# Optimization experiments

Measured on AMD Instinct MI355X. Metric: run time of the kernel, lower is better.

## Reference

```python
import jax, jax.numpy as jnp
import numpy as np

TEMP = 0.1
GROUPS = 16
EPS = 1e-5
COS_EPS = 1e-8


def _encoder(x, conv_w, conv_b, gn_g, gn_b):
    # Conv2d(C,C,3,pad=1) -> GroupNorm(16,C) -> ReLU -> AdaptiveAvgPool2d(1) -> Flatten
    y = jax.lax.conv_general_dilated(
        x, conv_w, window_strides=(1, 1), padding='SAME',
        dimension_numbers=('NCHW', 'OIHW', 'NCHW')) + conv_b[None, :, None, None]
    B, C, H, W = y.shape
    yg = y.reshape(B, GROUPS, C // GROUPS, H, W)
    mu = yg.mean(axis=(2, 3, 4), keepdims=True)
    var = yg.var(axis=(2, 3, 4), keepdims=True)
    yn = ((yg - mu) * jax.lax.rsqrt(var + EPS)).reshape(B, C, H, W)
    y = yn * gn_g[None, :, None, None] + gn_b[None, :, None, None]
    y = jax.nn.relu(y)
    return y.mean(axis=(2, 3))  # [B, C]


def _projector(h, w1, b1, w2, b2, ln_g, ln_b):
    h = jax.nn.relu(h @ w1 + b1)
    h = h @ w2 + b2
    mu = h.mean(axis=-1, keepdims=True)
    var = h.var(axis=-1, keepdims=True)
    return (h - mu) * jax.lax.rsqrt(var + EPS) * ln_g + ln_b


def _predictor(z, w1, b1, w2, b2):
    return jax.nn.relu(z @ w1 + b1) @ w2 + b2


def _l2norm(z):
    n = jnp.sqrt(jnp.sum(z * z, axis=1, keepdims=True))
    return z / jnp.maximum(n, COS_EPS)


def _pair_loss(zi, zj, off_idx):
    # vectorized version of the nested-loop cosine-sim + cross-entropy (label 0)
    S = (_l2norm(zi) @ _l2norm(zj).T) / TEMP  # [B, B]
    pos = jnp.diagonal(S)                     # sim(i_k, j_k)
    neg = jnp.take_along_axis(S, off_idx, axis=1)  # [B, B-1], row k = S[k, l!=k]
    logits = jnp.concatenate([pos[:, None], neg], axis=1)
    return jnp.mean(jax.nn.logsumexp(logits, axis=1) - logits[:, 0])


def setup_inputs() -> dict:
    key = jax.random.key(0)
    ks = jax.random.split(key, 32)
    B, C, H, W, P = 256, 256, 16, 16, 128
    d = {}
    d['x_t2w'] = jax.random.normal(ks[0], (B, C, H, W), jnp.float32)
    d['x_t2f'] = jax.random.normal(ks[1], (B, C, H, W), jnp.float32)
    d['x_t1n'] = jax.random.normal(ks[2], (B, C, H, W), jnp.float32)
    i = 3
    for m in ('t2w', 't2f', 't1n'):
        d[f'conv_w_{m}'] = jax.random.normal(ks[i], (C, C, 3, 3), jnp.float32) * 0.02; i += 1
        d[f'conv_b_{m}'] = jnp.zeros((C,), jnp.float32)
        d[f'gn_g_{m}'] = jnp.ones((C,), jnp.float32)
        d[f'gn_b_{m}'] = jnp.zeros((C,), jnp.float32)
    d['proj_w1'] = jax.random.normal(ks[i], (C, C), jnp.float32) * 0.02; i += 1
    d['proj_b1'] = jnp.zeros((C,), jnp.float32)
    d['proj_w2'] = jax.random.normal(ks[i], (C, P), jnp.float32) * 0.02; i += 1
    d['proj_b2'] = jnp.zeros((P,), jnp.float32)
    d['ln_g'] = jnp.ones((P,), jnp.float32)
    d['ln_b'] = jnp.zeros((P,), jnp.float32)
    d['pred_w1'] = jax.random.normal(ks[i], (P, P), jnp.float32) * 0.02; i += 1
    d['pred_b1'] = jnp.zeros((P,), jnp.float32)
    d['pred_w2'] = jax.random.normal(ks[i], (P, P), jnp.float32) * 0.02; i += 1
    d['pred_b2'] = jnp.zeros((P,), jnp.float32)
    return d


def reference(x_t2w, x_t2f, x_t1n,
              conv_w_t2w, conv_b_t2w, gn_g_t2w, gn_b_t2w,
              conv_w_t2f, conv_b_t2f, gn_g_t2f, gn_b_t2f,
              conv_w_t1n, conv_b_t1n, gn_g_t1n, gn_b_t1n,
              proj_w1, proj_b1, proj_w2, proj_b2, ln_g, ln_b,
              pred_w1, pred_b1, pred_w2, pred_b2):
    xs = [x_t2w, x_t2f, x_t1n]
    enc_params = [(conv_w_t2w, conv_b_t2w, gn_g_t2w, gn_b_t2w),
                  (conv_w_t2f, conv_b_t2f, gn_g_t2f, gn_b_t2f),
                  (conv_w_t1n, conv_b_t1n, gn_g_t1n, gn_b_t1n)]
    encoded = [_encoder(x, *p) for x, p in zip(xs, enc_params)]
    projected = [_projector(e, proj_w1, proj_b1, proj_w2, proj_b2, ln_g, ln_b) for e in encoded]
    preds = [_predictor(z, pred_w1, pred_b1, pred_w2, pred_b2) for z in projected]

    B = projected[0].shape[0]
    off_idx = jnp.asarray(np.array([[l for l in range(B) if l != k] for k in range(B)],
                                    dtype=np.int32))
    pairs = [(0, 1), (0, 2), (1, 2)]
    loss = sum(_pair_loss(projected[i], projected[j], off_idx) for i, j in pairs) / len(pairs)

    return (jnp.stack(encoded), jnp.stack(projected), jnp.stack(preds), loss)
```

## Files before the change

kernel.cpp:

```cpp
#include <hip/hip_runtime.h>
#include <hip/hip_bf16.h>

typedef float f32x4 __attribute__((ext_vector_type(4)));
typedef __bf16 bf16x8 __attribute__((ext_vector_type(8)));
typedef unsigned short u16x8 __attribute__((ext_vector_type(8)));

#define GN_EPS 1e-5f
#define LN_EPS 1e-5f
#define COS_EPS_F 1e-8f

__device__ __forceinline__ unsigned short f2bf(float f) {
  unsigned int u = __builtin_bit_cast(unsigned int, f);
  u += 0x7fffu + ((u >> 16) & 1u);
  return (unsigned short)(u >> 16);
}

__global__ void transpose_kernel(const float* __restrict__ x0,
                                 const float* __restrict__ x1,
                                 const float* __restrict__ x2,
                                 unsigned short* __restrict__ xT,
                                 unsigned int strideElems, int mBase) {
  __shared__ float lds[64][129];
  int m = mBase + (blockIdx.x >> 11);
  int bid = blockIdx.x & 2047;
  const float* x = (m == 0) ? x0 : ((m == 1) ? x1 : x2);
  unsigned short* dst = xT + (unsigned int)(m - mBase) * strideElems;

  int hwt = bid & 3, cit = (bid >> 2) & 1, b = bid >> 3;
  int hw0 = hwt * 64, ci0 = cit * 128;
  int tid = threadIdx.x;

  int hwx = tid & 63, cy0 = tid >> 6;
  const float* xb = x + (b * 256 + ci0) * 256 + hw0;
  #pragma unroll 8
  for (int p = 0; p < 32; ++p) {
    int cy = cy0 + 4 * p;
    lds[hwx][cy] = xb[cy * 256 + hwx];
  }
  __syncthreads();

  int cp = tid & 63, hy0 = tid >> 6;
  unsigned int* outp = (unsigned int*)(dst + (b * 256 + hw0) * 256 + ci0);
  #pragma unroll 4
  for (int p = 0; p < 16; ++p) {
    int hy = hy0 + 4 * p;
    float lo = lds[hy][2 * cp];
    float hi = lds[hy][2 * cp + 1];
    unsigned int w = ((unsigned int)f2bf(hi) << 16) | f2bf(lo);
    outp[hy * 128 + cp] = w;
  }
}

__global__ void pack_kernel(const float* __restrict__ w0,
                            const float* __restrict__ w1,
                            const float* __restrict__ w2,
                            unsigned short* __restrict__ wp) {
  int m = blockIdx.y;
  const float* w = (m == 0) ? w0 : ((m == 1) ? w1 : w2);
  int idx = blockIdx.x * 256 + threadIdx.x;
  int ci = idx & 255;
  int rest = idx >> 8;
  int khw = rest % 9, co = rest / 9;
  wp[m * 589824 + idx] = f2bf(w[(co * 256 + ci) * 9 + khw]);
}

__device__ __forceinline__ void gl_lds16(const unsigned short* g, unsigned short* l) {
  __builtin_amdgcn_global_load_lds(
      (const __attribute__((address_space(1))) void*)g,
      (__attribute__((address_space(3))) void*)l, 16, 0, 0);
}

__launch_bounds__(512, 2)
__global__ void conv_gn_pool(const unsigned short* __restrict__ xT,
                             unsigned int xTstride,
                             const unsigned short* __restrict__ wp,
                             const float* __restrict__ cb0, const float* __restrict__ cb1,
                             const float* __restrict__ cb2,
                             const float* __restrict__ gg0, const float* __restrict__ gg1,
                             const float* __restrict__ gg2,
                             const float* __restrict__ gb0, const float* __restrict__ gb1,
                             const float* __restrict__ gb2,
                             float* __restrict__ enc, int mBase, int chunk) {
  __shared__ unsigned short As[2][16384];
  __shared__ unsigned short Bb[3][4096];
  __shared__ unsigned short zbuf[32];
  __shared__ float gsum[16], gsq[16], pooled[256];

  int bid = blockIdx.x;
  int xcd = bid & 7, kk = bid >> 3;
  int nt = kk & 1;
  int pg = xcd * chunk + (kk >> 1);
  int mm = mBase + (pg >> 7);
  int pr = pg & 127;

  const float* cbias = (mm == 0) ? cb0 : ((mm == 1) ? cb1 : cb2);
  const float* gng   = (mm == 0) ? gg0 : ((mm == 1) ? gg1 : gg2);
  const float* gnb   = (mm == 0) ? gb0 : ((mm == 1) ? gb1 : gb2);

  int tid = threadIdx.x;
  int wid = tid >> 6, lane = tid & 63;
  int wr = wid >> 1, wc = wid & 1;
  int l15 = lane & 15, l4 = lane >> 4;

  if (tid < 16) { gsum[tid] = 0.f; gsq[tid] = 0.f; }
  if (tid < 256) pooled[tid] = 0.f;
  if (tid < 32) zbuf[tid] = 0;

  const unsigned short* xbPair =
      xT + (unsigned int)(mm - mBase) * xTstride + (unsigned int)(pr * 2) * 65536u;
  const unsigned short* wpB = wp + mm * 589824 + (nt * 128) * 2304;

  int sco = tid >> 2, sk4 = tid & 3;

  int hh8[8], ww8[8], bq8[8];
  #pragma unroll
  for (int mf = 0; mf < 8; ++mf) {
    int r = wr * 128 + mf * 16 + l15;
    int img = r >> 8, p = r & 255;
    hh8[mf] = p >> 4; ww8[mf] = p & 15;
    bq8[mf] = img * 8192 + p * 32 + l4 * 8;
  }
  int bq4[4];
  #pragma unroll
  for (int nf = 0; nf < 4; ++nf)
    bq4[nf] = (wc * 64 + nf * 16 + l15) * 32 + l4 * 8;

  f32x4 acc[8][4];
  #pragma unroll
  for (int i = 0; i < 8; ++i)
    #pragma unroll
    for (int j = 0; j < 4; ++j) acc[i][j] = (f32x4)(0.0f);

  #define LD8(P) __builtin_bit_cast(bf16x8, *(const u16x8*)(P))

  #define STAGE_A(KCN, PAR)                                                    \
    {                                                                          \
      unsigned short* dstA = &As[(PAR)][0];                                    \
      _Pragma("unroll")                                                        \
      for (int j = 0; j < 4; ++j) {                                            \
        int c = tid + j * 512;                                                 \
        int img_ = c >> 10, p_ = (c >> 2) & 255, k4_ = c & 3;                  \
        gl_lds16(xbPair + img_ * 65536 + p_ * 256 + (KCN) * 32 + k4_ * 8,      \
                 dstA + c * 8);                                                \
      }                                                                        \
    }
  #define STAGE_B(KC2, TAP2, BUF2)                                             \
    gl_lds16(wpB + sco * 2304 + (TAP2) * 256 + (KC2) * 32 + sk4 * 8,           \
             &Bb[(BUF2)][tid * 8]);

  #define TAP_BODY(TAP, DH, DW, DO_A, DO_B, KC2, TAP2, VMN)                    \
    {                                                                          \
      if (DO_A) STAGE_A(kc + 1, (kc + 1) & 1);                                 \
      if (DO_B) STAGE_B(KC2, TAP2, ((TAP) + 2) % 3);                           \
      const unsigned short* AsC = &As[kc & 1][0];                              \
      bf16x8 af[8], bfr[4];                                                    \
      _Pragma("unroll")                                                        \
      for (int nf = 0; nf < 4; ++nf)                                           \
        bfr[nf] = LD8(&Bb[(TAP) % 3][bq4[nf]]);                                \
      _Pragma("unroll")                                                        \
      for (int mf = 0; mf < 8; ++mf) {                                         \
        int ok = 1;                                                            \
        if ((DH) == 0) ok &= (hh8[mf] >= 1);                                   \
        if ((DH) == 2) ok &= (hh8[mf] <= 14);                                  \
        if ((DW) == 0) ok &= (ww8[mf] >= 1);                                   \
        if ((DW) == 2) ok &= (ww8[mf] <= 14);                                  \
        const unsigned short* pa =                                             \
            ok ? AsC + (bq8[mf] + (((DH) * 16 + (DW)) - 17) * 32)              \
               : &zbuf[l4 * 8];                                                \
        af[mf] = LD8(pa);                                                      \
      }                                                                        \
      __builtin_amdgcn_s_barrier();                                            \
      asm volatile("s_waitcnt lgkmcnt(0)" ::: "memory");                       \
      __builtin_amdgcn_sched_barrier(0);                                       \
      __builtin_amdgcn_s_setprio(1);                                           \
      _Pragma("unroll")                                                        \
      for (int mf = 0; mf < 8; ++mf)                                           \
        _Pragma("unroll")                                                      \
        for (int nf = 0; nf < 4; ++nf)                                         \
          acc[mf][nf] = __builtin_amdgcn_mfma_f32_16x16x32_bf16(               \
              af[mf], bfr[nf], acc[mf][nf], 0, 0, 0);                          \
      __builtin_amdgcn_s_setprio(0);                                           \
      asm volatile("s_waitcnt vmcnt(" #VMN ")" ::: "memory");                  \
      __builtin_amdgcn_s_barrier();                                            \
    }

  {
    int kc = 0; (void)kc;
    STAGE_A(0, 0);
    STAGE_B(0, 0, 0);
    STAGE_B(0, 1, 1);
    asm volatile("s_waitcnt vmcnt(1)" ::: "memory");
    __builtin_amdgcn_s_barrier();
  }

  for (int kc = 0; kc < 7; ++kc) {
    TAP_BODY(0, 0, 0, 1, 1, kc, 2, 5)
    TAP_BODY(1, 0, 1, 0, 1, kc, 3, 1)
    TAP_BODY(2, 0, 2, 0, 1, kc, 4, 1)
    TAP_BODY(3, 1, 0, 0, 1, kc, 5, 1)
    TAP_BODY(4, 1, 1, 0, 1, kc, 6, 1)
    TAP_BODY(5, 1, 2, 0, 1, kc, 7, 1)
    TAP_BODY(6, 2, 0, 0, 1, kc, 8, 1)
    TAP_BODY(7, 2, 1, 0, 1, kc + 1, 0, 1)
    TAP_BODY(8, 2, 2, 0, 1, kc + 1, 1, 1)
  }
  {
    const int kc = 7;
    TAP_BODY(0, 0, 0, 0, 1, 7, 2, 1)
    TAP_BODY(1, 0, 1, 0, 1, 7, 3, 1)
    TAP_BODY(2, 0, 2, 0, 1, 7, 4, 1)
    TAP_BODY(3, 1, 0, 0, 1, 7, 5, 1)
    TAP_BODY(4, 1, 1, 0, 1, 7, 6, 1)
    TAP_BODY(5, 1, 2, 0, 1, 7, 7, 1)
    TAP_BODY(6, 2, 0, 0, 1, 7, 8, 1)
    TAP_BODY(7, 2, 1, 0, 0, 7, 0, 0)
    TAP_BODY(8, 2, 2, 0, 0, 7, 0, 0)
  }
  #undef TAP_BODY
  #undef STAGE_A
  #undef STAGE_B
  #undef LD8

  __syncthreads();

  int img = wr >> 1;
  float bias[4], ggv[4], gbv[4];
  #pragma unroll
  for (int nf = 0; nf < 4; ++nf) {
    int co = nt * 128 + wc * 64 + nf * 16 + l15;
    bias[nf] = cbias[co]; ggv[nf] = gng[co]; gbv[nf] = gnb[co];
  }
  #pragma unroll
  for (int nf = 0; nf < 4; ++nf) {
    float s1 = 0.f, s2 = 0.f;
    #pragma unroll
    for (int mf = 0; mf < 8; ++mf)
      #pragma unroll
      for (int i = 0; i < 4; ++i) {
        float v = acc[mf][nf][i] + bias[nf];
        acc[mf][nf][i] = v;
        s1 += v; s2 += v * v;
      }
    #pragma unroll
    for (int d = 1; d < 64; d <<= 1) {
      s1 += __shfl_xor(s1, d);
      s2 += __shfl_xor(s2, d);
    }
    if (lane == 0) {
      atomicAdd(&gsum[img * 8 + wc * 4 + nf], s1);
      atomicAdd(&gsq[img * 8 + wc * 4 + nf], s2);
    }
  }
  __syncthreads();
  #pragma unroll
  for (int nf = 0; nf < 4; ++nf) {
    int g = img * 8 + wc * 4 + nf;
    float mean = gsum[g] * (1.f / 4096.f);
    float var = gsq[g] * (1.f / 4096.f) - mean * mean;
    float rs = rsqrtf(var + GN_EPS);
    float p = 0.f;
    #pragma unroll
    for (int mf = 0; mf < 8; ++mf)
      #pragma unroll
      for (int i = 0; i < 4; ++i) {
        float v = (acc[mf][nf][i] - mean) * rs * ggv[nf] + gbv[nf];
        p += fmaxf(v, 0.f);
      }
    p += __shfl_xor(p, 16);
    p += __shfl_xor(p, 32);
    if (lane < 16) atomicAdd(&pooled[img * 128 + wc * 64 + nf * 16 + l15], p);
  }
  __syncthreads();
  if (tid < 256) {
    int oimg = tid >> 7, ch = tid & 127;
    enc[mm * 65536 + (pr * 2 + oimg) * 256 + nt * 128 + ch] =
        pooled[tid] * (1.f / 256.f);
  }
}

__global__ void proj_pred(const float* __restrict__ enc,
                          const float* __restrict__ w1, const float* __restrict__ b1,
                          const float* __restrict__ w2, const float* __restrict__ b2,
                          const float* __restrict__ lng, const float* __restrict__ lnb,
                          const float* __restrict__ pw1, const float* __restrict__ pb1,
                          const float* __restrict__ pw2, const float* __restrict__ pb2,
                          float* __restrict__ proj, float* __restrict__ pred,
                          float* __restrict__ znorm) {
  __shared__ float row[256], h1[256], zz[128], p1[128], red[2];
  int r = blockIdx.x, tid = threadIdx.x;
  row[tid] = enc[r * 256 + tid];
  __syncthreads();
  float a = 0.f;
  for (int k = 0; k < 256; ++k) a += row[k] * w1[k * 256 + tid];
  h1[tid] = fmaxf(a + b1[tid], 0.f);
  __syncthreads();
  if (tid < 128) {
    a = 0.f;
    for (int k = 0; k < 256; ++k) a += h1[k] * w2[k * 128 + tid];
    zz[tid] = a + b2[tid];
  }
  __syncthreads();
  if (tid == 0) {
    float m = 0.f;
    for (int k = 0; k < 128; ++k) m += zz[k];
    m *= (1.f / 128.f);
    float v = 0.f;
    for (int k = 0; k < 128; ++k) { float d = zz[k] - m; v += d * d; }
    red[0] = m;
    red[1] = rsqrtf(v * (1.f / 128.f) + LN_EPS);
  }
  __syncthreads();
  float zval = 0.f;
  if (tid < 128) {
    zval = (zz[tid] - red[0]) * red[1] * lng[tid] + lnb[tid];
    proj[r * 128 + tid] = zval;
  }
  __syncthreads();
  if (tid < 128) zz[tid] = zval;
  __syncthreads();
  if (tid == 0) {
    float s = 0.f;
    for (int k = 0; k < 128; ++k) s += zz[k] * zz[k];
    red[0] = 1.f / fmaxf(sqrtf(s), COS_EPS_F);
  }
  __syncthreads();
  if (tid < 128) {
    znorm[r * 128 + tid] = zz[tid] * red[0];
    a = 0.f;
    for (int k = 0; k < 128; ++k) a += zz[k] * pw1[k * 128 + tid];
    p1[tid] = fmaxf(a + pb1[tid], 0.f);
  }
  __syncthreads();
  if (tid < 128) {
    a = 0.f;
    for (int k = 0; k < 128; ++k) a += p1[k] * pw2[k * 128 + tid];
    pred[r * 128 + tid] = a + pb2[tid];
  }
}

__global__ void loss_kernel(const float* __restrict__ zn, float* __restrict__ part) {
  __shared__ float zi[128], sv[256], rbuf[256];
  int blk = blockIdx.x;
  int p = blk >> 8, k = blk & 255;
  int i = (p == 2) ? 1 : 0;
  int j = (p == 0) ? 1 : 2;
  int tid = threadIdx.x;
  if (tid < 128) zi[tid] = zn[(i * 256 + k) * 128 + tid];
  __syncthreads();
  const float4* zj = (const float4*)&zn[(j * 256 + tid) * 128];
  float s = 0.f;
  #pragma unroll 8
  for (int d = 0; d < 32; ++d) {
    float4 aq = *(const float4*)&zi[d * 4];
    float4 bq = zj[d];
    s += aq.x * bq.x + aq.y * bq.y + aq.z * bq.z + aq.w * bq.w;
  }
  s *= 10.0f;
  sv[tid] = s;
  rbuf[tid] = s;
  __syncthreads();
  for (int d = 128; d > 0; d >>= 1) {
    if (tid < d) rbuf[tid] = fmaxf(rbuf[tid], rbuf[tid + d]);
    __syncthreads();
  }
  float m = rbuf[0];
  __syncthreads();
  rbuf[tid] = expf(s - m);
  __syncthreads();
  for (int d = 128; d > 0; d >>= 1) {
    if (tid < d) rbuf[tid] += rbuf[tid + d];
    __syncthreads();
  }
  if (tid == 0) part[blk] = m + logf(rbuf[0]) - sv[k];
}

__global__ void finalize_loss(const float* __restrict__ part, float* __restrict__ out) {
  __shared__ float red[256];
  int tid = threadIdx.x;
  float s = 0.f;
  for (int idx = tid; idx < 768; idx += 256) s += part[idx];
  red[tid] = s;
  __syncthreads();
  for (int d = 128; d > 0; d >>= 1) {
    if (tid < d) red[tid] += red[tid + d];
    __syncthreads();
  }
  if (tid == 0) out[0] = red[0] * (1.f / 768.f);
}

extern "C" void kernel_launch(void* const* d_in, const int* in_sizes, int n_in,
                              void* d_out, int out_size, void* d_ws, size_t ws_size,
                              hipStream_t stream) {
  const float* x[3]  = {(const float*)d_in[0], (const float*)d_in[1], (const float*)d_in[2]};
  const float* cw[3] = {(const float*)d_in[3], (const float*)d_in[7], (const float*)d_in[11]};
  const float* cb[3] = {(const float*)d_in[4], (const float*)d_in[8], (const float*)d_in[12]};
  const float* gg[3] = {(const float*)d_in[5], (const float*)d_in[9], (const float*)d_in[13]};
  const float* gb[3] = {(const float*)d_in[6], (const float*)d_in[10], (const float*)d_in[14]};
  const float* p_w1 = (const float*)d_in[15];
  const float* p_b1 = (const float*)d_in[16];
  const float* p_w2 = (const float*)d_in[17];
  const float* p_b2 = (const float*)d_in[18];
  const float* ln_g = (const float*)d_in[19];
  const float* ln_b = (const float*)d_in[20];
  const float* q_w1 = (const float*)d_in[21];
  const float* q_b1 = (const float*)d_in[22];
  const float* q_w2 = (const float*)d_in[23];
  const float* q_b2 = (const float*)d_in[24];

  float* out = (float*)d_out;
  char* ws = (char*)d_ws;

  const size_t XT_ONE = 33554432;
  bool merged = ws_size >= (3 * XT_ONE + 3538944 + 393216 + 3072 + 512);

  size_t xt_total = merged ? 3 * XT_ONE : XT_ONE;
  unsigned short* xT  = (unsigned short*)ws;
  unsigned short* wpk = (unsigned short*)(ws + xt_total);
  float* znorm = (float*)(ws + xt_total + 3538944);
  float* part  = (float*)(ws + xt_total + 3538944 + 393216);

  float* enc  = out;
  float* proj = out + 196608;
  float* pred = out + 294912;
  float* lossp = out + 393216;

  pack_kernel<<<dim3(2304, 3), dim3(256), 0, stream>>>(cw[0], cw[1], cw[2], wpk);

  if (merged) {
    transpose_kernel<<<dim3(6144), dim3(256), 0, stream>>>(x[0], x[1], x[2], xT, 16777216u, 0);
    conv_gn_pool<<<dim3(768), dim3(512), 0, stream>>>(
        xT, 16777216u, wpk, cb[0], cb[1], cb[2], gg[0], gg[1], gg[2],
        gb[0], gb[1], gb[2], enc, 0, 48);
  } else {
    for (int m = 0; m < 3; ++m) {
      transpose_kernel<<<dim3(2048), dim3(256), 0, stream>>>(x[0], x[1], x[2], xT, 0u, m);
      conv_gn_pool<<<dim3(256), dim3(512), 0, stream>>>(
          xT, 0u, wpk, cb[0], cb[1], cb[2], gg[0], gg[1], gg[2],
          gb[0], gb[1], gb[2], enc, m, 16);
    }
  }
  proj_pred<<<dim3(768), dim3(256), 0, stream>>>(enc, p_w1, p_b1, p_w2, p_b2, ln_g, ln_b,
                                                 q_w1, q_b1, q_w2, q_b2, proj, pred, znorm);
  loss_kernel<<<dim3(768), dim3(256), 0, stream>>>(znorm, part);
  finalize_loss<<<dim3(1), dim3(256), 0, stream>>>(part, lossp);
}
```

Baseline: 343.9 us.

## Shrink conv workgroup to one image, load weights directly to registers

The conv+GroupNorm+pool kernel now uses 256-thread workgroups that each handle one image and half of the output channels, instead of 512 threads covering two images. Weight fragments are prefetched straight from global memory into double-buffered registers rather than staged through LDS, and the A tile in LDS uses an XOR swizzle to avoid bank conflicts. Per-tap barriers and priority tweaks are removed, leaving one barrier per K chunk. The trade-off is less weight reuse across images, more global weight traffic and exposed register-load latency, in exchange for twice as many workgroups and smaller LDS use.

```diff
diff --git a/kernel.cpp b/kernel.cpp
--- a/kernel.cpp
+++ b/kernel.cpp
@@ -70,7 +70,7 @@
       (__attribute__((address_space(3))) void*)l, 16, 0, 0);
 }
 
-__launch_bounds__(512, 2)
+__launch_bounds__(256, 2)
 __global__ void conv_gn_pool(const unsigned short* __restrict__ xT,
                              unsigned int xTstride,
                              const unsigned short* __restrict__ wp,
@@ -80,19 +80,16 @@
                              const float* __restrict__ gg2,
                              const float* __restrict__ gb0, const float* __restrict__ gb1,
                              const float* __restrict__ gb2,
-                             float* __restrict__ enc, int mBase, int chunk) {
-  __shared__ unsigned short As[2][16384];
-  __shared__ unsigned short Bb[3][4096];
+                             float* __restrict__ enc, int mBase, int cpx) {
+  __shared__ unsigned short As[2][8192];
   __shared__ unsigned short zbuf[32];
-  __shared__ float gsum[16], gsq[16], pooled[256];
+  __shared__ float gsum[8], gsq[8], pooled[128];
 
   int bid = blockIdx.x;
-  int xcd = bid & 7, kk = bid >> 3;
-  int nt = kk & 1;
-  int pg = xcd * chunk + (kk >> 1);
-  int mm = mBase + (pg >> 7);
-  int pr = pg & 127;
-
+  int wgid = (bid & 7) * cpx + (bid >> 3);
+  int mm = mBase + (wgid >> 9);
+  int rest = wgid & 511;
+  int img = rest >> 1, nt = rest & 1;
   const float* cbias = (mm == 0) ? cb0 : ((mm == 1) ? cb1 : cb2);
   const float* gng   = (mm == 0) ? gg0 : ((mm == 1) ? gg1 : gg2);
   const float* gnb   = (mm == 0) ? gb0 : ((mm == 1) ? gb1 : gb2);
@@ -102,28 +99,38 @@
   int wr = wid >> 1, wc = wid & 1;
   int l15 = lane & 15, l4 = lane >> 4;
 
-  if (tid < 16) { gsum[tid] = 0.f; gsq[tid] = 0.f; }
-  if (tid < 256) pooled[tid] = 0.f;
+  if (tid < 8) { gsum[tid] = 0.f; gsq[tid] = 0.f; }
+  if (tid < 128) pooled[tid] = 0.f;
   if (tid < 32) zbuf[tid] = 0;
 
-  const unsigned short* xbPair =
-      xT + (unsigned int)(mm - mBase) * xTstride + (unsigned int)(pr * 2) * 65536u;
-  const unsigned short* wpB = wp + mm * 589824 + (nt * 128) * 2304;
-
-  int sco = tid >> 2, sk4 = tid & 3;
-
-  int hh8[8], ww8[8], bq8[8];
+  const unsigned short* xb =
+      xT + (unsigned int)(mm - mBase) * xTstride + (unsigned int)img * 65536u;
+  const unsigned short* wpB = wp + mm * 589824 + nt * 128 * 2304;
+
+  const unsigned short* aS[4];
+  #pragma unroll
+  for (int j = 0; j < 4; ++j) {
+    int c = j * 256 + tid;
+    int r = c >> 2, ch = c & 3;
+    aS[j] = xb + r * 256 + ((ch ^ ((r >> 1) & 3)) * 8);
+  }
+
+  const unsigned short* bP[4];
+  #pragma unroll
+  for (int nf = 0; nf < 4; ++nf) {
+    int co = wc * 64 + nf * 16 + l15;
+    bP[nf] = wpB + co * 2304 + l4 * 8;
+  }
+
+  int p8[8];
+  bool hge1[8], hle14[8], wge1[8], wle14[8];
   #pragma unroll
   for (int mf = 0; mf < 8; ++mf) {
-    int r = wr * 128 + mf * 16 + l15;
-    int img = r >> 8, p = r & 255;
-    hh8[mf] = p >> 4; ww8[mf] = p & 15;
-    bq8[mf] = img * 8192 + p * 32 + l4 * 8;
-  }
-  int bq4[4];
-  #pragma unroll
-  for (int nf = 0; nf < 4; ++nf)
-    bq4[nf] = (wc * 64 + nf * 16 + l15) * 32 + l4 * 8;
+    int p = wr * 128 + mf * 16 + l15;
+    p8[mf] = p;
+    hge1[mf] = (p >> 4) >= 1;  hle14[mf] = (p >> 4) <= 14;
+    wge1[mf] = (p & 15) >= 1;  wle14[mf] = (p & 15) <= 14;
+  }
 
   f32x4 acc[8][4];
   #pragma unroll
@@ -132,98 +139,69 @@
     for (int j = 0; j < 4; ++j) acc[i][j] = (f32x4)(0.0f);
 
   #define LD8(P) __builtin_bit_cast(bf16x8, *(const u16x8*)(P))
-
-  #define STAGE_A(KCN, PAR)                                                    \
+  #define STAGE_A(KCN, BUF)                                                    \
+    { _Pragma("unroll")                                                        \
+      for (int j = 0; j < 4; ++j)                                              \
+        gl_lds16(aS[j] + (KCN) * 32, As[BUF] + (j * 256 + tid) * 8); }
+
+  u16x8 Pb[4], Qb[4];
+  #define PF(REGS, TAPN)                                                       \
+    { _Pragma("unroll")                                                        \
+      for (int nf = 0; nf < 4; ++nf)                                           \
+        REGS[nf] = *(const u16x8*)(bP[nf] + kco + (TAPN) * 256); }
+
+  #define TAP(DH, DW, CUR, NXT, PFT)                                           \
     {                                                                          \
-      unsigned short* dstA = &As[(PAR)][0];                                    \
-      _Pragma("unroll")                                                        \
-      for (int j = 0; j < 4; ++j) {                                            \
-        int c = tid + j * 512;                                                 \
-        int img_ = c >> 10, p_ = (c >> 2) & 255, k4_ = c & 3;                  \
-        gl_lds16(xbPair + img_ * 65536 + p_ * 256 + (KCN) * 32 + k4_ * 8,      \
-                 dstA + c * 8);                                                \
-      }                                                                        \
-    }
-  #define STAGE_B(KC2, TAP2, BUF2)                                             \
-    gl_lds16(wpB + sco * 2304 + (TAP2) * 256 + (KC2) * 32 + sk4 * 8,           \
-             &Bb[(BUF2)][tid * 8]);
-
-  #define TAP_BODY(TAP, DH, DW, DO_A, DO_B, KC2, TAP2, VMN)                    \
-    {                                                                          \
-      if (DO_A) STAGE_A(kc + 1, (kc + 1) & 1);                                 \
-      if (DO_B) STAGE_B(KC2, TAP2, ((TAP) + 2) % 3);                           \
-      const unsigned short* AsC = &As[kc & 1][0];                              \
-      bf16x8 af[8], bfr[4];                                                    \
-      _Pragma("unroll")                                                        \
-      for (int nf = 0; nf < 4; ++nf)                                           \
-        bfr[nf] = LD8(&Bb[(TAP) % 3][bq4[nf]]);                                \
+      if ((PFT) >= 0) PF(NXT, PFT);                                            \
+      bf16x8 af[8];                                                            \
       _Pragma("unroll")                                                        \
       for (int mf = 0; mf < 8; ++mf) {                                         \
-        int ok = 1;                                                            \
-        if ((DH) == 0) ok &= (hh8[mf] >= 1);                                   \
-        if ((DH) == 2) ok &= (hh8[mf] <= 14);                                  \
-        if ((DW) == 0) ok &= (ww8[mf] >= 1);                                   \
-        if ((DW) == 2) ok &= (ww8[mf] <= 14);                                  \
+        int pp = p8[mf] + ((DH) - 1) * 16 + ((DW) - 1);                        \
+        bool ok = true;                                                        \
+        if ((DH) == 0) ok = ok && hge1[mf];                                    \
+        if ((DH) == 2) ok = ok && hle14[mf];                                   \
+        if ((DW) == 0) ok = ok && wge1[mf];                                    \
+        if ((DW) == 2) ok = ok && wle14[mf];                                   \
         const unsigned short* pa =                                             \
-            ok ? AsC + (bq8[mf] + (((DH) * 16 + (DW)) - 17) * 32)              \
+            ok ? AsC + (pp * 32 + ((l4 ^ ((pp >> 1) & 3)) * 8))                \
                : &zbuf[l4 * 8];                                                \
         af[mf] = LD8(pa);                                                      \
       }                                                                        \
-      __builtin_amdgcn_s_barrier();                                            \
-      asm volatile("s_waitcnt lgkmcnt(0)" ::: "memory");                       \
-      __builtin_amdgcn_sched_barrier(0);                                       \
-      __builtin_amdgcn_s_setprio(1);                                           \
       _Pragma("unroll")                                                        \
       for (int mf = 0; mf < 8; ++mf)                                           \
         _Pragma("unroll")                                                      \
         for (int nf = 0; nf < 4; ++nf)                                         \
           acc[mf][nf] = __builtin_amdgcn_mfma_f32_16x16x32_bf16(               \
-              af[mf], bfr[nf], acc[mf][nf], 0, 0, 0);                          \
-      __builtin_amdgcn_s_setprio(0);                                           \
-      asm volatile("s_waitcnt vmcnt(" #VMN ")" ::: "memory");                  \
-      __builtin_amdgcn_s_barrier();                                            \
+              af[mf], __builtin_bit_cast(bf16x8, CUR[nf]), acc[mf][nf],        \
+              0, 0, 0);                                                        \
     }
 
-  {
-    int kc = 0; (void)kc;
-    STAGE_A(0, 0);
-    STAGE_B(0, 0, 0);
-    STAGE_B(0, 1, 1);
-    asm volatile("s_waitcnt vmcnt(1)" ::: "memory");
+  STAGE_A(0, 0);
+  asm volatile("s_waitcnt vmcnt(0)" ::: "memory");
+  __builtin_amdgcn_s_barrier();
+
+  for (int kc = 0; kc < 8; ++kc) {
+    if (kc < 7) STAGE_A(kc + 1, (kc + 1) & 1);
+    const unsigned short* AsC = As[kc & 1];
+    int kco = kc * 32;
+    PF(Pb, 0);
+    TAP(0, 0, Pb, Qb, 1)
+    TAP(0, 1, Qb, Pb, 2)
+    TAP(0, 2, Pb, Qb, 3)
+    TAP(1, 0, Qb, Pb, 4)
+    TAP(1, 1, Pb, Qb, 5)
+    TAP(1, 2, Qb, Pb, 6)
+    TAP(2, 0, Pb, Qb, 7)
+    TAP(2, 1, Qb, Pb, 8)
+    TAP(2, 2, Pb, Qb, -1)
+    asm volatile("s_waitcnt vmcnt(0)" ::: "memory");
     __builtin_amdgcn_s_barrier();
   }
-
-  for (int kc = 0; kc < 7; ++kc) {
-    TAP_BODY(0, 0, 0, 1, 1, kc, 2, 5)
-    TAP_BODY(1, 0, 1, 0, 1, kc, 3, 1)
-    TAP_BODY(2, 0, 2, 0, 1, kc, 4, 1)
-    TAP_BODY(3, 1, 0, 0, 1, kc, 5, 1)
-    TAP_BODY(4, 1, 1, 0, 1, kc, 6, 1)
-    TAP_BODY(5, 1, 2, 0, 1, kc, 7, 1)
-    TAP_BODY(6, 2, 0, 0, 1, kc, 8, 1)
-    TAP_BODY(7, 2, 1, 0, 1, kc + 1, 0, 1)
-    TAP_BODY(8, 2, 2, 0, 1, kc + 1, 1, 1)
-  }
-  {
-    const int kc = 7;
-    TAP_BODY(0, 0, 0, 0, 1, 7, 2, 1)
-    TAP_BODY(1, 0, 1, 0, 1, 7, 3, 1)
-    TAP_BODY(2, 0, 2, 0, 1, 7, 4, 1)
-    TAP_BODY(3, 1, 0, 0, 1, 7, 5, 1)
-    TAP_BODY(4, 1, 1, 0, 1, 7, 6, 1)
-    TAP_BODY(5, 1, 2, 0, 1, 7, 7, 1)
-    TAP_BODY(6, 2, 0, 0, 1, 7, 8, 1)
-    TAP_BODY(7, 2, 1, 0, 0, 7, 0, 0)
-    TAP_BODY(8, 2, 2, 0, 0, 7, 0, 0)
-  }
-  #undef TAP_BODY
+  #undef TAP
+  #undef PF
   #undef STAGE_A
-  #undef STAGE_B
   #undef LD8
 
-  __syncthreads();
-
-  int img = wr >> 1;
   float bias[4], ggv[4], gbv[4];
   #pragma unroll
   for (int nf = 0; nf < 4; ++nf) {
@@ -247,14 +225,14 @@
       s2 += __shfl_xor(s2, d);
     }
     if (lane == 0) {
-      atomicAdd(&gsum[img * 8 + wc * 4 + nf], s1);
-      atomicAdd(&gsq[img * 8 + wc * 4 + nf], s2);
+      atomicAdd(&gsum[wc * 4 + nf], s1);
+      atomicAdd(&gsq[wc * 4 + nf], s2);
     }
   }
   __syncthreads();
   #pragma unroll
   for (int nf = 0; nf < 4; ++nf) {
-    int g = img * 8 + wc * 4 + nf;
+    int g = wc * 4 + nf;
     float mean = gsum[g] * (1.f / 4096.f);
     float var = gsq[g] * (1.f / 4096.f) - mean * mean;
     float rs = rsqrtf(var + GN_EPS);
@@ -268,14 +246,11 @@
       }
     p += __shfl_xor(p, 16);
     p += __shfl_xor(p, 32);
-    if (lane < 16) atomicAdd(&pooled[img * 128 + wc * 64 + nf * 16 + l15], p);
-  }
-  __syncthreads();
-  if (tid < 256) {
-    int oimg = tid >> 7, ch = tid & 127;
-    enc[mm * 65536 + (pr * 2 + oimg) * 256 + nt * 128 + ch] =
-        pooled[tid] * (1.f / 256.f);
-  }
+    if (lane < 16) atomicAdd(&pooled[wc * 64 + nf * 16 + l15], p);
+  }
+  __syncthreads();
+  if (tid < 128)
+    enc[mm * 65536 + img * 256 + nt * 128 + tid] = pooled[tid] * (1.f / 256.f);
 }
 
 __global__ void proj_pred(const float* __restrict__ enc,
@@ -411,7 +386,7 @@
   char* ws = (char*)d_ws;
 
   const size_t XT_ONE = 33554432;
-  bool merged = ws_size >= (3 * XT_ONE + 3538944 + 393216 + 3072 + 512);
+  bool merged = ws_size >= (3 * XT_ONE + 3538944 + 393216 + 3072);
 
   size_t xt_total = merged ? 3 * XT_ONE : XT_ONE;
   unsigned short* xT  = (unsigned short*)ws;
@@ -428,15 +403,15 @@
 
   if (merged) {
     transpose_kernel<<<dim3(6144), dim3(256), 0, stream>>>(x[0], x[1], x[2], xT, 16777216u, 0);
-    conv_gn_pool<<<dim3(768), dim3(512), 0, stream>>>(
+    conv_gn_pool<<<dim3(1536), dim3(256), 0, stream>>>(
         xT, 16777216u, wpk, cb[0], cb[1], cb[2], gg[0], gg[1], gg[2],
-        gb[0], gb[1], gb[2], enc, 0, 48);
+        gb[0], gb[1], gb[2], enc, 0, 192);
   } else {
     for (int m = 0; m < 3; ++m) {
       transpose_kernel<<<dim3(2048), dim3(256), 0, stream>>>(x[0], x[1], x[2], xT, 0u, m);
-      conv_gn_pool<<<dim3(256), dim3(512), 0, stream>>>(
+      conv_gn_pool<<<dim3(512), dim3(256), 0, stream>>>(
           xT, 0u, wpk, cb[0], cb[1], cb[2], gg[0], gg[1], gg[2],
-          gb[0], gb[1], gb[2], enc, m, 16);
+          gb[0], gb[1], gb[2], enc, m, 64);
     }
   }
   proj_pred<<<dim3(768), dim3(256), 0, stream>>>(enc, p_w1, p_b1, p_w2, p_b2, ln_g, ln_b,
```

New measurement: 692.3 us. 2.01x slower.
